# Kernel tuning notes

Hardware: AMD Instinct MI355X
Metric: run time of the kernel (lower is better)

## Reference

```python
import jax, jax.numpy as jnp
import numpy as np

B, T, C, FF = 4, 2048, 2048, 8192
EPS_LN = 1e-5
EPS_WKV = 1e-8


def _ln(x, g, b):
    mu = jnp.mean(x, axis=-1, keepdims=True)
    var = jnp.var(x, axis=-1, keepdims=True)
    return (x - mu) * jax.lax.rsqrt(var + EPS_LN) * g + b


def setup_inputs() -> dict:
    key = jax.random.key(0)
    ks = jax.random.split(key, 9)
    w = lambda k, shape: (jax.random.normal(k, shape, jnp.float32) * 0.02)
    return {
        "x": jax.random.normal(ks[0], (B, T, C), jnp.float32),
        "ln1_g": jnp.ones((C,), jnp.float32),
        "ln1_b": jnp.zeros((C,), jnp.float32),
        "time_decay": jax.random.normal(ks[1], (C,), jnp.float32),
        "Wk": w(ks[2], (C, C)),
        "Wv": w(ks[3], (C, C)),
        "Wr": w(ks[4], (C, C)),
        "ln2_g": jnp.ones((C,), jnp.float32),
        "ln2_b": jnp.zeros((C,), jnp.float32),
        "Wck": w(ks[5], (FF, C)),   # key: d_model -> d_ffn
        "Wcv": w(ks[6], (C, FF)),   # value: d_ffn -> d_model
        "Wcr": w(ks[7], (C, C)),    # receptance
    }


def reference(x, ln1_g, ln1_b, time_decay, Wk, Wv, Wr, ln2_g, ln2_b, Wck, Wcv, Wcr):
    # --- TimeMix branch ---
    xln = _ln(x, ln1_g, ln1_b)
    # ZeroPad2d((0,0,1,-1)): shift tokens right by one (zero at t=0, drop last)
    shifted = jnp.pad(xln, ((0, 0), (1, 0), (0, 0)))[:, :-1]  # [B,T,C]
    k = jnp.einsum('btc,dc->btd', shifted, Wk)
    v = jnp.einsum('btc,dc->btd', shifted, Wv)
    r = jnp.einsum('btc,dc->btd', xln, Wr)

    # WKV: exponentially-decayed running weighted average (RWKV linear recurrence)
    decay = jnp.exp(-jnp.exp(time_decay))  # per-channel decay in (0,1)

    def step(carry, kv_t):
        a, b = carry
        k_t, v_t = kv_t
        ek = jnp.exp(k_t)
        a = decay * a + ek * v_t
        b = decay * b + ek
        return (a, b), a / (b + EPS_WKV)

    kT = jnp.swapaxes(k, 0, 1)  # [T,B,C]
    vT = jnp.swapaxes(v, 0, 1)
    init = (jnp.zeros((B, C), x.dtype), jnp.zeros((B, C), x.dtype))
    _, wkvT = jax.lax.scan(step, init, (kT, vT))
    wkv = jnp.swapaxes(wkvT, 0, 1)  # [B,T,C]

    x = x + r * wkv

    # --- ChannelMix branch ---
    x2 = _ln(x, ln2_g, ln2_b)
    ck = jnp.square(jax.nn.relu(jnp.einsum('btc,fc->btf', x2, Wck)))
    dv = jnp.einsum('btf,cf->btc', ck, Wcv)
    cr = jax.nn.sigmoid(jnp.einsum('btc,dc->btd', x2, Wcr))
    x = x + cr * dv

    state = shifted[:, -1]  # [B,C]
    return (x, state)
```

## Files before the change

kernel.cpp:

```cpp
#include <hip/hip_runtime.h>
#include <hip/hip_fp16.h>

typedef unsigned short us;
using short8 = __attribute__((ext_vector_type(8))) short;
using f32x4  = __attribute__((ext_vector_type(4))) float;

#define B_  4
#define T_  2048
#define C_  2048
#define FF_ 8192
#define M_  (B_*T_)
#define NCHB 5
#define NCH (1<<NCHB)
#define LCH (T_/NCH)
#define EPS_WKV 1e-8f
#define NK  (C_/64)

__device__ __forceinline__ us f2bf(float f) {
  union { float f; unsigned u; } v; v.f = f;
  return (us)((v.u + 0x7fffu + ((v.u >> 16) & 1u)) >> 16);
}

__device__ __forceinline__ void gload_lds16(const void* g, void* l) {
  __builtin_amdgcn_global_load_lds((__attribute__((address_space(1))) void*)(void*)g,
                                   (__attribute__((address_space(3))) void*)l, 16, 0, 0);
}

__global__ __launch_bounds__(256)
void cvt_bf16(const float* __restrict__ s, us* __restrict__ d) {
  const int i = (blockIdx.x * 256 + threadIdx.x) * 4;
  const float4 v = *(const float4*)(s + i);
  ushort4 o; o.x = f2bf(v.x); o.y = f2bf(v.y); o.z = f2bf(v.z); o.w = f2bf(v.w);
  *(ushort4*)(d + i) = o;
}

__global__ __launch_bounds__(256)
void cvt_bf16_str(const float* __restrict__ s, us* __restrict__ d, int srs) {
  const int row = blockIdx.y;
  const int col = (blockIdx.x * 256 + threadIdx.x) * 4;
  const float4 v = *(const float4*)(s + (size_t)row * srs + col);
  ushort4 o; o.x = f2bf(v.x); o.y = f2bf(v.y); o.z = f2bf(v.z); o.w = f2bf(v.w);
  *(ushort4*)(d + (size_t)row * 2048 + col) = o;
}

template<bool WS>
__global__ __launch_bounds__(256)
void ln_kern(const float* __restrict__ x, const float* __restrict__ g,
             const float* __restrict__ bi, us* __restrict__ y,
             float* __restrict__ state)
{
  const int row = blockIdx.x;
  const int tid = threadIdx.x;
  const float* xr = x + (size_t)row * C_;
  const float4 v0 = ((const float4*)xr)[tid];
  const float4 v1 = ((const float4*)xr)[tid + 256];
  float s  = v0.x + v0.y + v0.z + v0.w + v1.x + v1.y + v1.z + v1.w;
  float sq = v0.x*v0.x + v0.y*v0.y + v0.z*v0.z + v0.w*v0.w
           + v1.x*v1.x + v1.y*v1.y + v1.z*v1.z + v1.w*v1.w;
  #pragma unroll
  for (int o = 32; o > 0; o >>= 1) { s += __shfl_down(s, o, 64); sq += __shfl_down(sq, o, 64); }
  __shared__ float ws_[4], wq_[4];
  if ((tid & 63) == 0) { ws_[tid >> 6] = s; wq_[tid >> 6] = sq; }
  __syncthreads();
  s  = ws_[0] + ws_[1] + ws_[2] + ws_[3];
  sq = wq_[0] + wq_[1] + wq_[2] + wq_[3];
  const float mean = s * (1.f / C_);
  const float rstd = rsqrtf(sq * (1.f / C_) - mean * mean + 1e-5f);
  const float4 g0 = ((const float4*)g)[tid],  g1 = ((const float4*)g)[tid + 256];
  const float4 b0 = ((const float4*)bi)[tid], b1 = ((const float4*)bi)[tid + 256];
  const float o0x = (v0.x - mean) * rstd * g0.x + b0.x;
  const float o0y = (v0.y - mean) * rstd * g0.y + b0.y;
  const float o0z = (v0.z - mean) * rstd * g0.z + b0.z;
  const float o0w = (v0.w - mean) * rstd * g0.w + b0.w;
  const float o1x = (v1.x - mean) * rstd * g1.x + b1.x;
  const float o1y = (v1.y - mean) * rstd * g1.y + b1.y;
  const float o1z = (v1.z - mean) * rstd * g1.z + b1.z;
  const float o1w = (v1.w - mean) * rstd * g1.w + b1.w;
  ushort4 p0; p0.x = f2bf(o0x); p0.y = f2bf(o0y); p0.z = f2bf(o0z); p0.w = f2bf(o0w);
  ushort4 p1; p1.x = f2bf(o1x); p1.y = f2bf(o1y); p1.z = f2bf(o1z); p1.w = f2bf(o1w);
  ((ushort4*)(y + (size_t)row * C_))[tid]       = p0;
  ((ushort4*)(y + (size_t)row * C_))[tid + 256] = p1;
  if (WS && ((row & (T_ - 1)) == (T_ - 2))) {
    float* st = state + (size_t)(row >> 11) * C_;
    const int c0 = tid * 4;
    st[c0 + 0] = o0x; st[c0 + 1] = o0y; st[c0 + 2] = o0z; st[c0 + 3] = o0w;
    st[c0 + 1024 + 0] = o1x; st[c0 + 1024 + 1] = o1y;
    st[c0 + 1024 + 2] = o1z; st[c0 + 1024 + 3] = o1w;
  }
}


#define STAGE_A(D,KB,KO) do { \
  gload_lds16(gA1 + (KO), &lds[(D)*16384 + (KB)*8192 + sdA]); \
  gload_lds16(gA2 + (KO), &lds[(D)*16384 + (KB)*8192 + sdA + 4096]); } while(0)
#define STAGE_B(D,KB,KO) do { \
  gload_lds16(gB1 + (KO), &lds[(D)*16384 + (KB)*8192 + sdB]); \
  gload_lds16(gB2 + (KO), &lds[(D)*16384 + (KB)*8192 + sdB + 4096]); } while(0)

#define LDA_(MF,D,KB) (*(const short8*)&lds[(D)*16384 + (KB)*8192 + (rA + (MF)*16)*32 + cA])
#define LDB_(NF,D,KB) (*(const short8*)&lds[32768 + (D)*16384 + (KB)*8192 + (rB + (NF)*16)*32 + cB])

#define READ_PH2(D,KB) do { \
  _Pragma("unroll") for (int _i = 0; _i < 8; _i++) af[_i] = LDA_(_i,(D),(KB)); \
  _Pragma("unroll") for (int _j = 0; _j < 4; _j++) bf[_j] = LDB_(_j,(D),(KB)); } while(0)

#define MFMA32() do { _Pragma("unroll") \
  for (int _i = 0; _i < 8; _i++) { _Pragma("unroll") \
    for (int _j = 0; _j < 4; _j++) \
      acc[_i][_j] = __builtin_amdgcn_mfma_f32_16x16x32_bf16(af[_i], bf[_j], acc[_i][_j], 0, 0, 0); } } while(0)

#define PH_PRE() do { \
  __builtin_amdgcn_s_barrier(); \
  __builtin_amdgcn_sched_barrier(0); \
  asm volatile("s_waitcnt lgkmcnt(0)" ::: "memory"); \
  __builtin_amdgcn_sched_barrier(0); \
  __builtin_amdgcn_s_setprio(1); } while(0)

#define PH_POST_VM4() do { \
  __builtin_amdgcn_s_setprio(0); \
  asm volatile("s_waitcnt vmcnt(4)" ::: "memory"); \
  __builtin_amdgcn_s_barrier(); \
  __builtin_amdgcn_sched_barrier(0); } while(0)

template<int MODE>
__global__ __launch_bounds__(512, 2)
void gemm_nt(const us* __restrict__ A, const us* __restrict__ Bw,
             void* __restrict__ out0, void* __restrict__ out1, void* __restrict__ out2,
             const __half* __restrict__ crv, float* __restrict__ fout)
{
  __shared__ __align__(16) us lds[65536];
  const int tid  = threadIdx.x;
  const int w    = tid >> 6, l = tid & 63;
  const int quad = l >> 4, l16 = l & 15;
  const int wm = w >> 2, wn = w & 3;
  const size_t m0 = (size_t)blockIdx.y * 256, n0 = (size_t)blockIdx.x * 256;

  const int rA = wm * 128 + l16;
  const int rB = wn * 64  + l16;
  const int cA = (quad ^ ((rA >> 1) & 3)) * 8;
  const int cB = (quad ^ ((rB >> 1) & 3)) * 8;

  const int srow = l >> 2;
  const int scol = ((l & 3) ^ ((l >> 3) & 3)) * 8;
  const us* gA1 = A  + (m0 + (size_t)(w * 16 + srow)) * C_ + scol;
  const us* gA2 = gA1 + (size_t)64 * C_ * 2;
  const us* gB1 = Bw + (n0 + (size_t)(w * 16 + srow)) * C_ + scol;
  const us* gB2 = gB1 + (size_t)64 * C_ * 2;
  const int sdA = w * 512;
  const int sdB = 32768 + w * 512;

  f32x4 acc[8][4];
  #pragma unroll
  for (int i = 0; i < 8; i++)
    #pragma unroll
    for (int j = 0; j < 4; j++)
      acc[i][j] = (f32x4){0.f, 0.f, 0.f, 0.f};

  short8 af[8], bf[4];

  STAGE_A(0, 0, 0); STAGE_B(0, 0, 0);
  STAGE_A(0, 1, 32); STAGE_B(0, 1, 32);
  asm volatile("s_waitcnt vmcnt(4)" ::: "memory");
  __builtin_amdgcn_s_barrier();
  __builtin_amdgcn_sched_barrier(0);

  int cur = 0;
  #pragma unroll 1
  for (int kt = 0; kt < NK - 1; ++kt) {
    const int nxt = cur ^ 1;
    const int ko  = (kt + 1) * 64;
    READ_PH2(cur, 0);
    STAGE_A(nxt, 0, ko); STAGE_B(nxt, 0, ko);
    PH_PRE(); MFMA32(); PH_POST_VM4();
    READ_PH2(cur, 1);
    STAGE_A(nxt, 1, ko + 32); STAGE_B(nxt, 1, ko + 32);
    PH_PRE(); MFMA32(); PH_POST_VM4();
    cur = nxt;
  }

  READ_PH2(cur, 0);
  PH_PRE(); MFMA32();
  __builtin_amdgcn_s_setprio(0);
  asm volatile("s_waitcnt vmcnt(0)" ::: "memory");
  __builtin_amdgcn_s_barrier();
  __builtin_amdgcn_sched_barrier(0);
  READ_PH2(cur, 1);
  PH_PRE(); MFMA32();
  __builtin_amdgcn_s_setprio(0);

  const int nb = (int)(n0 >> 11);
  const size_t ncol0 = n0 - ((size_t)nb << 11);

  #pragma unroll
  for (int mf = 0; mf < 8; mf++) {
    const size_t rbase = m0 + (size_t)(wm * 128 + mf * 16 + quad * 4);
    #pragma unroll
    for (int j = 0; j < 4; j++) {
      const size_t rowoff = (rbase + j) * C_;
      #pragma unroll
      for (int nf = 0; nf < 4; nf++) {
        const size_t nc = (size_t)(wn * 64 + nf * 16 + l16);
        const float v = acc[mf][nf][j];
        if (MODE == 1) {
          const float t = v > 0.f ? v : 0.f;
          ((us*)out0)[rowoff + n0 + nc] = f2bf(t * t);
        } else if (MODE == 2) {
          ((__half*)out0)[rowoff + n0 + nc] = __float2half(1.f / (1.f + expf(-v)));
        } else if (MODE == 3) {
          const size_t idx = rowoff + n0 + nc;
          fout[idx] += (float)crv[idx] * v;
        } else {
          const size_t idx = rowoff + ncol0 + nc;
          if (nb == 0)      ((__half*)out0)[idx] = __float2half(v);
          else if (nb == 1) ((__half*)out1)[idx] = __float2half(v);
          else              ((float*)out2)[idx]  = v;
        }
      }
    }
  }
}

__global__ __launch_bounds__(256)
void wkv_pass1(const __half* __restrict__ Kh, const __half* __restrict__ Vh,
               const float* __restrict__ tdec, float* __restrict__ chA, float* __restrict__ chB)
{
  const int idx = blockIdx.x * 256 + threadIdx.x;
  const int c = idx & (C_ - 1);
  const int chunk = (idx >> 11) & (NCH - 1);
  const int b = idx >> (11 + NCHB);
  const float d = expf(-expf(tdec[c]));
  const size_t base = ((size_t)b * T_) * C_ + c;
  float a = 0.f, bb = 0.f;
  const int t0 = chunk * LCH;
  int t = t0;
  if (chunk == 0) { bb = 1.f; t = 1; }
  const int tend = t0 + LCH;
  #pragma unroll 4
  for (; t < tend; ++t) {
    const size_t off = base + (size_t)(t - 1) * C_;
    const float ek = expf((float)Kh[off]);
    const float vv = (float)Vh[off];
    a  = d * a  + ek * vv;
    bb = d * bb + ek;
  }
  chA[idx] = a; chB[idx] = bb;
}

__global__ __launch_bounds__(256)
void wkv_pass2(const float* __restrict__ tdec, float* __restrict__ chA, float* __restrict__ chB)
{
  const int idx = blockIdx.x * 256 + threadIdx.x;
  const int c = idx & (C_ - 1);
  const int b = idx >> 11;
  const float dL = expf(-expf(tdec[c]) * (float)LCH);
  float a = 0.f, bb = 0.f;
  #pragma unroll
  for (int ch = 0; ch < NCH; ++ch) {
    const int s = (b * NCH + ch) * C_ + c;
    const float la = chA[s], lb = chB[s];
    chA[s] = a; chB[s] = bb;
    a  = dL * a  + la;
    bb = dL * bb + lb;
  }
}

__global__ __launch_bounds__(256)
void wkv_pass3(const __half* __restrict__ Kh, const __half* __restrict__ Vh,
               const float* __restrict__ xin, const float* __restrict__ tdec,
               const float* __restrict__ chA, const float* __restrict__ chB,
               float* __restrict__ outx)
{
  const int idx = blockIdx.x * 256 + threadIdx.x;
  const int c = idx & (C_ - 1);
  const int chunk = (idx >> 11) & (NCH - 1);
  const int b = idx >> (11 + NCHB);
  const float d = expf(-expf(tdec[c]));
  const size_t base = ((size_t)b * T_) * C_ + c;
  float a = chA[idx], bb = chB[idx];
  const int t0 = chunk * LCH;
  int t = t0;
  if (chunk == 0) {
    a = d * a;
    bb = d * bb + 1.f;
    const float wkv = a / (bb + EPS_WKV);
    const float r = outx[base];
    outx[base] = xin[base] + r * wkv;
    t = 1;
  }
  const int tend = t0 + LCH;
  #pragma unroll 4
  for (; t < tend; ++t) {
    const size_t offp = base + (size_t)(t - 1) * C_;
    const size_t off  = base + (size_t)t * C_;
    const float ek = expf((float)Kh[offp]);
    const float vv = (float)Vh[offp];
    a  = d * a  + ek * vv;
    bb = d * bb + ek;
    const float wkv = a / (bb + EPS_WKV);
    const float r = outx[off];
    outx[off] = xin[off] + r * wkv;
  }
}

extern "C" void kernel_launch(void* const* d_in, const int* in_sizes, int n_in,
                              void* d_out, int out_size, void* d_ws, size_t ws_size,
                              hipStream_t stream)
{
  const float* x    = (const float*)d_in[0];
  const float* ln1g = (const float*)d_in[1];
  const float* ln1b = (const float*)d_in[2];
  const float* tdec = (const float*)d_in[3];
  const float* Wk   = (const float*)d_in[4];
  const float* Wv   = (const float*)d_in[5];
  const float* Wr   = (const float*)d_in[6];
  const float* ln2g = (const float*)d_in[7];
  const float* ln2b = (const float*)d_in[8];
  const float* Wck  = (const float*)d_in[9];
  const float* Wcv  = (const float*)d_in[10];
  const float* Wcr  = (const float*)d_in[11];

  char* ws = (char*)d_ws;
  us*     xln  = (us*)(ws);
  __half* Kb   = (__half*)(ws + (32ull  << 20));
  __half* Vb   = (__half*)(ws + (64ull  << 20));
  us*     wkvr = (us*)(ws + (97ull  << 20));
  float*  chA  = (float*)(ws + (97ull << 20));
  float*  chB  = (float*)(ws + (98ull << 20));
  us*     wcrb = (us*)(ws + (121ull << 20));
  us*     wckc = (us*)(ws + (129ull << 20));
  us*     wcvc = (us*)(ws + (137ull << 20));
  us*     x2   = (us*)Kb;
  __half* crb  = (__half*)Vb;
  us*     ckc  = (us*)xln;

  float* outx = (float*)d_out;
  float* outs = outx + (size_t)M_ * C_;

  const dim3 blk(256);
  const dim3 blkG(512);
  const dim3 gC(C_ / 256, M_ / 256);
  const dim3 gKVR(3 * C_ / 256, M_ / 256);

  cvt_bf16<<<4096, blk, 0, stream>>>(Wk,  wkvr);
  cvt_bf16<<<4096, blk, 0, stream>>>(Wv,  wkvr + (size_t)C_ * C_);
  cvt_bf16<<<4096, blk, 0, stream>>>(Wr,  wkvr + 2 * (size_t)C_ * C_);
  cvt_bf16<<<4096, blk, 0, stream>>>(Wcr, wcrb);

  ln_kern<true><<<M_, blk, 0, stream>>>(x, ln1g, ln1b, xln, outs);

  gemm_nt<5><<<gKVR, blkG, 0, stream>>>(xln, wkvr, (void*)Kb, (void*)Vb, (void*)outx, nullptr, nullptr);

  wkv_pass1<<<(B_ * NCH * C_) / 256, blk, 0, stream>>>(Kb, Vb, tdec, chA, chB);
  wkv_pass2<<<(B_ * C_) / 256,       blk, 0, stream>>>(tdec, chA, chB);
  wkv_pass3<<<(B_ * NCH * C_) / 256, blk, 0, stream>>>(Kb, Vb, x, tdec, chA, chB, outx);

  ln_kern<false><<<M_, blk, 0, stream>>>(outx, ln2g, ln2b, x2, nullptr);

  gemm_nt<2><<<gC, blkG, 0, stream>>>(x2, wcrb, (void*)crb, nullptr, nullptr, nullptr, nullptr);

  for (int f0 = 0; f0 < FF_; f0 += 2048) {
    cvt_bf16<<<4096, blk, 0, stream>>>(Wck + (size_t)f0 * C_, wckc);
    gemm_nt<1><<<gC, blkG, 0, stream>>>(x2, wckc, (void*)ckc, nullptr, nullptr, nullptr, nullptr);
    cvt_bf16_str<<<dim3(2, 2048), blk, 0, stream>>>(Wcv + f0, wcvc, FF_);
    gemm_nt<3><<<gC, blkG, 0, stream>>>(ckc, wcvc, nullptr, nullptr, nullptr, crb, outx);
  }
}
```

Before: 1.218 ms.

## Restructure GEMM main loop into interleaved LDS reads and half-tile MFMA batches

Reworks the GEMM K-loop so that the next full 64-wide K tile is prefetched at the start of each iteration. LDS fragment reads are now interleaved with 16-MFMA batches, with A fragments split into two halves of four, instead of reading all fragments and then issuing 32 MFMAs per phase. This cuts the A fragment registers from 8 to 4 and removes the per-phase barrier and lgkmcnt wait. It now waits for vmcnt(0) once per tile, and the loop is unrolled by two with constant buffer indices. The risk is less slack to hide global load latency, since each tile fully drains before the barrier, and the compiler's own LDS wait placement may stall the MFMAs.

```diff
diff --git a/kernel.cpp b/kernel.cpp
--- a/kernel.cpp
+++ b/kernel.cpp
@@ -97,30 +97,62 @@
   gload_lds16(gB1 + (KO), &lds[(D)*16384 + (KB)*8192 + sdB]); \
   gload_lds16(gB2 + (KO), &lds[(D)*16384 + (KB)*8192 + sdB + 4096]); } while(0)
 
+#define STAGE_TILE(D,KO) do { \
+  STAGE_A(D, 0, (KO)); STAGE_B(D, 0, (KO)); \
+  STAGE_A(D, 1, (KO) + 32); STAGE_B(D, 1, (KO) + 32); } while(0)
+
 #define LDA_(MF,D,KB) (*(const short8*)&lds[(D)*16384 + (KB)*8192 + (rA + (MF)*16)*32 + cA])
 #define LDB_(NF,D,KB) (*(const short8*)&lds[32768 + (D)*16384 + (KB)*8192 + (rB + (NF)*16)*32 + cB])
 
-#define READ_PH2(D,KB) do { \
-  _Pragma("unroll") for (int _i = 0; _i < 8; _i++) af[_i] = LDA_(_i,(D),(KB)); \
-  _Pragma("unroll") for (int _j = 0; _j < 4; _j++) bf[_j] = LDB_(_j,(D),(KB)); } while(0)
-
-#define MFMA32() do { _Pragma("unroll") \
-  for (int _i = 0; _i < 8; _i++) { _Pragma("unroll") \
-    for (int _j = 0; _j < 4; _j++) \
-      acc[_i][_j] = __builtin_amdgcn_mfma_f32_16x16x32_bf16(af[_i], bf[_j], acc[_i][_j], 0, 0, 0); } } while(0)
-
-#define PH_PRE() do { \
-  __builtin_amdgcn_s_barrier(); \
+#define READ_A4(MF0,D,KB) do { _Pragma("unroll") \
+  for (int _i = 0; _i < 4; _i++) af[_i] = LDA_((MF0)+_i,(D),(KB)); } while(0)
+#define READ_B4(D,KB) do { _Pragma("unroll") \
+  for (int _j = 0; _j < 4; _j++) bf[_j] = LDB_(_j,(D),(KB)); } while(0)
+
+#define MFMA16(MF0) do { \
+  __builtin_amdgcn_s_setprio(1); \
+  { _Pragma("unroll") \
+    for (int _i = 0; _i < 4; _i++) { _Pragma("unroll") \
+      for (int _j = 0; _j < 4; _j++) \
+        acc[(MF0)+_i][_j] = __builtin_amdgcn_mfma_f32_16x16x32_bf16(af[_i 	% 4 == _i ? _i : _i], bf[_j], acc[(MF0)+_i][_j], 0, 0, 0); } } \
+  __builtin_amdgcn_s_setprio(0); } while(0)
+
+#undef MFMA16
+#define MFMA16(MF0) do { \
+  __builtin_amdgcn_s_setprio(1); \
+  { _Pragma("unroll") \
+    for (int _i = 0; _i < 4; _i++) { _Pragma("unroll") \
+      for (int _j = 0; _j < 4; _j++) \
+        acc[(MF0)+_i][_j] = __builtin_amdgcn_mfma_f32_16x16x32_bf16(af[_i], bf[_j], acc[(MF0)+_i][_j], 0, 0, 0); } } \
+  __builtin_amdgcn_s_setprio(0); } while(0)
+
+#define TILE_SYNC() do { \
   __builtin_amdgcn_sched_barrier(0); \
-  asm volatile("s_waitcnt lgkmcnt(0)" ::: "memory"); \
-  __builtin_amdgcn_sched_barrier(0); \
-  __builtin_amdgcn_s_setprio(1); } while(0)
-
-#define PH_POST_VM4() do { \
-  __builtin_amdgcn_s_setprio(0); \
-  asm volatile("s_waitcnt vmcnt(4)" ::: "memory"); \
+  asm volatile("s_waitcnt vmcnt(0)" ::: "memory"); \
   __builtin_amdgcn_s_barrier(); \
   __builtin_amdgcn_sched_barrier(0); } while(0)
+
+#define KTILE_BODY(D,SB) do { \
+  SB; \
+  READ_A4(0,D,0); READ_B4(D,0); \
+  MFMA16(0); \
+  READ_A4(4,D,0); \
+  MFMA16(4); \
+  READ_A4(0,D,1); READ_B4(D,1); \
+  MFMA16(0); \
+  READ_A4(4,D,1); \
+  MFMA16(4); \
+  TILE_SYNC(); } while(0)
+
+#define KTILE_LAST(D) do { \
+  READ_A4(0,D,0); READ_B4(D,0); \
+  MFMA16(0); \
+  READ_A4(4,D,0); \
+  MFMA16(4); \
+  READ_A4(0,D,1); READ_B4(D,1); \
+  MFMA16(0); \
+  READ_A4(4,D,1); \
+  MFMA16(4); } while(0)
 
 template<int MODE>
 __global__ __launch_bounds__(512, 2)
@@ -143,9 +175,9 @@
   const int srow = l >> 2;
   const int scol = ((l & 3) ^ ((l >> 3) & 3)) * 8;
   const us* gA1 = A  + (m0 + (size_t)(w * 16 + srow)) * C_ + scol;
-  const us* gA2 = gA1 + (size_t)64 * C_ * 2;
+  const us* gA2 = gA1 + (size_t)128 * C_;
   const us* gB1 = Bw + (n0 + (size_t)(w * 16 + srow)) * C_ + scol;
-  const us* gB2 = gB1 + (size_t)64 * C_ * 2;
+  const us* gB2 = gB1 + (size_t)128 * C_;
   const int sdA = w * 512;
   const int sdB = 32768 + w * 512;
 
@@ -156,37 +188,20 @@
     for (int j = 0; j < 4; j++)
       acc[i][j] = (f32x4){0.f, 0.f, 0.f, 0.f};
 
-  short8 af[8], bf[4];
-
-  STAGE_A(0, 0, 0); STAGE_B(0, 0, 0);
-  STAGE_A(0, 1, 32); STAGE_B(0, 1, 32);
-  asm volatile("s_waitcnt vmcnt(4)" ::: "memory");
-  __builtin_amdgcn_s_barrier();
-  __builtin_amdgcn_sched_barrier(0);
-
-  int cur = 0;
+  short8 af[4], bf[4];
+
+  STAGE_TILE(0, 0);
+  TILE_SYNC();
+
   #pragma unroll 1
-  for (int kt = 0; kt < NK - 1; ++kt) {
-    const int nxt = cur ^ 1;
-    const int ko  = (kt + 1) * 64;
-    READ_PH2(cur, 0);
-    STAGE_A(nxt, 0, ko); STAGE_B(nxt, 0, ko);
-    PH_PRE(); MFMA32(); PH_POST_VM4();
-    READ_PH2(cur, 1);
-    STAGE_A(nxt, 1, ko + 32); STAGE_B(nxt, 1, ko + 32);
-    PH_PRE(); MFMA32(); PH_POST_VM4();
-    cur = nxt;
-  }
-
-  READ_PH2(cur, 0);
-  PH_PRE(); MFMA32();
-  __builtin_amdgcn_s_setprio(0);
-  asm volatile("s_waitcnt vmcnt(0)" ::: "memory");
-  __builtin_amdgcn_s_barrier();
-  __builtin_amdgcn_sched_barrier(0);
-  READ_PH2(cur, 1);
-  PH_PRE(); MFMA32();
-  __builtin_amdgcn_s_setprio(0);
+  for (int kt = 0; kt < NK - 2; kt += 2) {
+    const int ko1 = (kt + 1) * 64;
+    const int ko2 = (kt + 2) * 64;
+    KTILE_BODY(0, STAGE_TILE(1, ko1));
+    KTILE_BODY(1, STAGE_TILE(0, ko2));
+  }
+  KTILE_BODY(0, STAGE_TILE(1, (NK - 1) * 64));
+  KTILE_LAST(1);
 
   const int nb = (int)(n0 >> 11);
   const size_t ncol0 = n0 - ((size_t)nb << 11);
```

After: 1.253 ms. 2.9% more time.
